# Kernel tuning notes

Measured on AMD Instinct MI355X. Metric: run time of the kernel, lower is better.

## Reference

```python
import jax, jax.numpy as jnp
import numpy as np

B, N, K = 32, 64, 128          # batch, atoms per cell, channel width (128x0e + 128x1o)
R_MAX = 5.0
NUM_BESSEL = 8
P_CUT = 5                       # num_polynomial_cutoff
AVG_NEIGH = 16.0                # avg_num_neighbors
H_MLP = 512                     # hidden_dimensions_size, n_hidden_dimensions = 2
FEAT = 5 * K                    # ((num_interactions-1)*4 + 1) * 128 = 640


def silu(x):
    return x * jax.nn.sigmoid(x)


def _bessel_cutoff(r, mask):
    # Bessel radial basis * polynomial cutoff (MACE), masked on valid edges.
    n = jnp.arange(1, NUM_BESSEL + 1, dtype=r.dtype)
    rb = jnp.sqrt(2.0 / R_MAX) * jnp.sin(n * (jnp.pi / R_MAX) * r[..., None]) / r[..., None]
    u = r / R_MAX
    p = float(P_CUT)
    fc = 1.0 - 0.5 * (p + 1) * (p + 2) * u**P_CUT + p * (p + 2) * u**(P_CUT + 1) - 0.5 * p * (p + 1) * u**(P_CUT + 2)
    fc = fc * (u < 1.0)
    return rb * (fc * mask)[..., None]


def _sph(uvec):
    # Real spherical harmonics l=0,1,2 (component normalization), uvec: unit edge vectors.
    x, y, z = uvec[..., 0], uvec[..., 1], uvec[..., 2]
    s3, s5, s15 = 3.0**0.5, 5.0**0.5, 15.0**0.5
    Y0 = jnp.ones_like(x)[..., None]
    Y1 = jnp.stack([s3 * x, s3 * y, s3 * z], -1)
    Y2 = jnp.stack([s15 * x * y, s15 * y * z, 0.5 * s5 * (3 * z * z - 1.0),
                    s15 * x * z, 0.5 * s15 * (x * x - y * y)], -1)
    return Y0, Y1, Y2


def _radial_mlp(x, w0, b0, w1, b1, w2, b2, w3, b3):
    h = silu(x @ w0 + b0)
    h = silu(h @ w1 + b1)
    h = silu(h @ w2 + b2)
    return h @ w3 + b3


def setup_inputs() -> dict:
    key = jax.random.key(0)
    ks = jax.random.split(key, 32)
    f32 = jnp.float32

    def lin(k, fan_in, shape):
        return (jax.random.normal(k, shape, dtype=f32) / np.sqrt(fan_in)).astype(f32)

    inp = {
        "noisy_relative_positions": jax.random.uniform(ks[0], (B, N, 3), dtype=f32),
        "time": jax.random.uniform(ks[1], (B, 1), dtype=f32),
        "unit_cell": (11.0 * jnp.eye(3, dtype=f32) + 0.3 * jax.random.uniform(ks[2], (B, 3, 3), dtype=f32)),
        "w_embed": lin(ks[3], 1, (K,)),
        # interaction 1 radial MLP: 8 -> 64 -> 64 -> 64 -> 3*K (weights for l=0,1,2 paths)
        "r1_w0": lin(ks[4], NUM_BESSEL, (NUM_BESSEL, 64)), "r1_b0": jnp.zeros((64,), f32),
        "r1_w1": lin(ks[5], 64, (64, 64)), "r1_b1": jnp.zeros((64,), f32),
        "r1_w2": lin(ks[6], 64, (64, 64)), "r1_b2": jnp.zeros((64,), f32),
        "r1_w3": lin(ks[7], 64, (64, 3 * K)), "r1_b3": jnp.zeros((3 * K,), f32),
        "mix1_l0": lin(ks[8], K, (K, K)),
        "mix1_l1": lin(ks[9], K, (K, K)),
        "mix1_l2": lin(ks[10], K, (K, K)),
        # interaction 2 radial MLP: 8 -> 64 -> 64 -> 64 -> 2*K (paths 0e x 0e -> 0e, 1o x 1o -> 0e)
        "r2_w0": lin(ks[11], NUM_BESSEL, (NUM_BESSEL, 64)), "r2_b0": jnp.zeros((64,), f32),
        "r2_w1": lin(ks[12], 64, (64, 64)), "r2_b1": jnp.zeros((64,), f32),
        "r2_w2": lin(ks[13], 64, (64, 64)), "r2_b2": jnp.zeros((64,), f32),
        "r2_w3": lin(ks[14], 64, (64, 2 * K)), "r2_b3": jnp.zeros((2 * K,), f32),
        "mix2": lin(ks[15], K, (K, K)),
        # readout MLP: 641 -> 512 -> 512 -> 3
        "mlp_w0": lin(ks[16], FEAT + 1, (FEAT + 1, H_MLP)), "mlp_b0": jnp.zeros((H_MLP,), f32),
        "mlp_w1": lin(ks[17], H_MLP, (H_MLP, H_MLP)), "mlp_b1": jnp.zeros((H_MLP,), f32),
        "mlp_w2": lin(ks[18], H_MLP, (H_MLP, 3)), "mlp_b2": jnp.zeros((3,), f32),
    }
    return inp


def reference(noisy_relative_positions, time, unit_cell, w_embed,
              r1_w0, r1_b0, r1_w1, r1_b1, r1_w2, r1_b2, r1_w3, r1_b3,
              mix1_l0, mix1_l1, mix1_l2,
              r2_w0, r2_b0, r2_w1, r2_b1, r2_w2, r2_b2, r2_w3, r2_b3, mix2,
              mlp_w0, mlp_b0, mlp_w1, mlp_b1, mlp_w2, mlp_b2):
    frac = noisy_relative_positions                      # [B,N,3] fractional
    d = frac[:, :, None, :] - frac[:, None, :, :]        # [B,N,N,3]
    d = d - jnp.round(d)                                 # minimum-image PBC
    dc = jnp.einsum('bijc,bcd->bijd', d, unit_cell)      # cartesian displacements
    r = jnp.sqrt(jnp.maximum(jnp.sum(dc * dc, -1), 1e-12))
    mask = (r < R_MAX) & (~jnp.eye(N, dtype=bool))[None]
    r_safe = jnp.where(mask, r, 1.0)
    uvec = dc / r_safe[..., None] * mask[..., None]      # unit edge vectors (0 off-edge)

    rad = _bessel_cutoff(r_safe, mask)                   # [B,N,N,8]
    Y0, Y1, Y2 = _sph(uvec)                              # [B,N,N,1|3|5]

    h0 = jnp.broadcast_to(w_embed, (B, N, K))            # element embedding (single species)

    # ---- interaction 1: radial-weighted tensor product h_j (x) Y_l, scatter over j ----
    we = _radial_mlp(rad, r1_w0, r1_b0, r1_w1, r1_b1, r1_w2, r1_b2, r1_w3, r1_b3)
    we = we.reshape(B, N, N, 3, K) * mask[..., None, None]
    hj = h0[:, None, :, :]                               # sender features [B,1,N,K]
    msg0 = jnp.einsum('bijk,bijm->bimk', we[..., 0, :] * hj, Y0)[:, :, 0] / AVG_NEIGH  # [B,N,K]
    msg1 = jnp.einsum('bijk,bijm->bimk', we[..., 1, :] * hj, Y1) / AVG_NEIGH           # [B,N,3,K]
    msg2 = jnp.einsum('bijk,bijm->bimk', we[..., 2, :] * hj, Y2) / AVG_NEIGH           # [B,N,5,K]

    s1 = msg0 @ mix1_l0 + jnp.sum(msg2 * msg2, axis=2) @ mix1_l2   # scalars [B,N,K]
    v1 = jnp.einsum('bimk,kc->bimc', msg1, mix1_l1)                # vectors [B,N,3,K]
    h1 = silu(s1)

    # ---- interaction 2: scalar output from 0e x 0e and 1o x 1o -> 0e paths ----
    we2 = _radial_mlp(rad, r2_w0, r2_b0, r2_w1, r2_b1, r2_w2, r2_b2, r2_w3, r2_b3)
    we2 = we2.reshape(B, N, N, 2, K) * mask[..., None, None]
    msg_a = jnp.sum(we2[..., 0, :] * h1[:, None, :, :], axis=2)    # [B,N,K]
    inv = jnp.einsum('bijm,bjmk->bijk', Y1, v1)                    # Y1 . v1_j invariant
    msg_b = jnp.sum(we2[..., 1, :] * inv, axis=2)
    s2 = ((msg_a + msg_b) / AVG_NEIGH) @ mix2                      # [B,N,K]

    # node_feats: layer1 full irreps (128x0e + 128x1o -> 512) + layer2 scalars (128) = 640
    node_feats = jnp.concatenate([s1, v1.reshape(B, N, 3 * K), s2], axis=-1)

    t = jnp.broadcast_to(time[:, None, :], (B, N, 1))
    x = jnp.concatenate([node_feats, t], axis=-1)                  # [B,N,641]
    x = jax.nn.relu(x @ mlp_w0 + mlp_b0)
    x = jax.nn.relu(x @ mlp_w1 + mlp_b1)
    return x @ mlp_w2 + mlp_b2                                     # [B,N,3]
```

## Files before the change

kernel.cpp:

```cpp
#include <hip/hip_runtime.h>
#include <math.h>

#define B_ 32
#define N_ 64
#define K_ 128
#define NPAIR (B_*N_*N_)
#define PREP_TOTAL 733184

typedef __attribute__((ext_vector_type(8))) short short8;
typedef __attribute__((ext_vector_type(8))) __bf16 bf16x8;
typedef __attribute__((ext_vector_type(4))) float floatx4;

__device__ __forceinline__ float silu_f(float x) {
    return x / (1.0f + expf(-x));
}

__device__ __forceinline__ short f2bf(float x) {
    union { float f; unsigned u; } v; v.f = x;
    unsigned r = (v.u + 0x7FFFu + ((v.u >> 16) & 1u)) >> 16;
    return (short)r;
}
__device__ __forceinline__ float bf2f(short s) {
    union { unsigned u; float f; } v;
    v.u = ((unsigned)(unsigned short)s) << 16;
    return v.f;
}
__device__ __forceinline__ bf16x8 ld_frag(const short* p) {
    short8 r = *(const short8*)p;
    return __builtin_bit_cast(bf16x8, r);
}

__global__ __launch_bounds__(256) void prep_kernel(
    const float* __restrict__ r1w1, const float* __restrict__ r1w2,
    const float* __restrict__ r2w1, const float* __restrict__ r2w2,
    const float* __restrict__ r2w3, const float* __restrict__ mw0,
    const float* __restrict__ mw1,
    const float* __restrict__ r1w0, const float* __restrict__ r2w0,
    const float* __restrict__ r1w3,
    const float* __restrict__ l0, const float* __restrict__ l1,
    const float* __restrict__ l2,
    short* __restrict__ dst)
{
    int idx = blockIdx.x * 256 + threadIdx.x;
    if (idx >= PREP_TOTAL) return;
    short v;
    if (idx < 4096) {
        int h = idx >> 6, k = idx & 63; v = f2bf(r1w1[k*64 + h]);
    } else if (idx < 8192) {
        int i = idx - 4096; int h = i >> 6, k = i & 63; v = f2bf(r1w2[k*64 + h]);
    } else if (idx < 12288) {
        int i = idx - 8192; int h = i >> 6, k = i & 63; v = f2bf(r2w1[k*64 + h]);
    } else if (idx < 16384) {
        int i = idx - 12288; int h = i >> 6, k = i & 63; v = f2bf(r2w2[k*64 + h]);
    } else if (idx < 32768) {
        int i = idx - 16384; int col = i >> 6, h = i & 63; v = f2bf(r2w3[h*256 + col]);
    } else if (idx < 393216) {
        int i = idx - 32768; int n = i / 704, k = i - n*704;
        v = (k < 641) ? f2bf(mw0[(size_t)k*512 + n]) : (short)0;
    } else if (idx < 655360) {
        int i = idx - 393216; int n = i >> 9, k = i & 511;
        v = f2bf(mw1[(size_t)k*512 + n]);
    } else if (idx < 657408) {
        int i = idx - 655360; int h = i >> 5, k = i & 31;
        v = (k < 8) ? f2bf(r1w0[k*64 + h]) : (short)0;
    } else if (idx < 659456) {
        int i = idx - 657408; int h = i >> 5, k = i & 31;
        v = (k < 8) ? f2bf(r2w0[k*64 + h]) : (short)0;
    } else if (idx < 684032) {
        int i = idx - 659456; int col = i >> 6, h = i & 63;
        v = f2bf(r1w3[(size_t)h*384 + col]);
    } else {
        int i = idx - 684032; int n = i >> 7, k = i & 127;
        float src = (n < 128) ? l0[(size_t)k*128 + n]
                  : (n < 256) ? l1[(size_t)k*128 + (n-128)]
                              : l2[(size_t)k*128 + (n-256)];
        v = f2bf(src);
    }
    dst[idx] = v;
}

__global__ __launch_bounds__(256) void geom_kernel(
    const float* __restrict__ pos, const float* __restrict__ cell,
    float* __restrict__ rad, float* __restrict__ Y1, float* __restrict__ Y2,
    float* __restrict__ maskf)
{
    int p = blockIdx.x * 256 + threadIdx.x;
    if (p >= NPAIR) return;
    int b = p >> 12;
    int ij = p & 4095;
    int i = ij >> 6, j = ij & 63;
    const float* pi = pos + (size_t)(b*N_ + i)*3;
    const float* pj = pos + (size_t)(b*N_ + j)*3;
    float d0 = pi[0]-pj[0], d1 = pi[1]-pj[1], d2 = pi[2]-pj[2];
    d0 -= rintf(d0); d1 -= rintf(d1); d2 -= rintf(d2);
    const float* C = cell + b*9;
    float dc0 = d0*C[0] + d1*C[3] + d2*C[6];
    float dc1 = d0*C[1] + d1*C[4] + d2*C[7];
    float dc2 = d0*C[2] + d1*C[5] + d2*C[8];
    float r2 = fmaxf(dc0*dc0 + dc1*dc1 + dc2*dc2, 1e-12f);
    float r = sqrtf(r2);
    bool m = (r < 5.0f) && (i != j);
    float mf = m ? 1.0f : 0.0f;
    float rs = m ? r : 1.0f;
    float inv_rs = 1.0f / rs;
    float x = dc0*inv_rs*mf, y = dc1*inv_rs*mf, z = dc2*inv_rs*mf;
    float u = r * 0.2f;
    float u2 = u*u, u4 = u2*u2, u5 = u4*u;
    float fc = 1.0f - 21.0f*u5 + 35.0f*u5*u - 15.0f*u5*u2;
    fc = (u < 1.0f) ? fc : 0.0f;
    float pref = 0.6324555320336759f * inv_rs * (fc * mf);
    float w = 0.6283185307179586f * rs;
    float sw = sinf(w), cw = cosf(w);
    float twoc = 2.0f * cw;
    float sm = 0.0f, s = sw;
    #pragma unroll
    for (int n = 1; n <= 8; n++) {
        rad[(size_t)p*8 + (n-1)] = pref * s;
        float nx = twoc*s - sm;
        sm = s; s = nx;
    }
    const float s3  = 1.7320508075688772f;
    const float s5  = 2.23606797749979f;
    const float s15 = 3.872983346207417f;
    float* y1 = Y1 + (size_t)p*3;
    y1[0] = s3*x; y1[1] = s3*y; y1[2] = s3*z;
    float* y2 = Y2 + (size_t)p*5;
    y2[0] = s15*x*y;
    y2[1] = s15*y*z;
    y2[2] = 0.5f*s5*(3.0f*z*z - 1.0f);
    y2[3] = s15*x*z;
    y2[4] = 0.5f*s15*(x*x - y*y);
    maskf[p] = mf;
}

__device__ __forceinline__ void mfma_layer(
    const short* __restrict__ src, const short* __restrict__ WT,
    const float* __restrict__ bias, short* __restrict__ dst,
    int wv, int qd, int nn)
{
    floatx4 acc[4];
    #pragma unroll
    for (int tt = 0; tt < 4; tt++) acc[tt] = (floatx4){0.f, 0.f, 0.f, 0.f};
    #pragma unroll
    for (int ks = 0; ks < 64; ks += 32) {
        bf16x8 a = ld_frag(&src[(wv*16 + nn)*72 + ks + qd*8]);
        #pragma unroll
        for (int tt = 0; tt < 4; tt++) {
            bf16x8 b = ld_frag(&WT[(tt*16 + nn)*64 + ks + qd*8]);
            acc[tt] = __builtin_amdgcn_mfma_f32_16x16x32_bf16(a, b, acc[tt], 0, 0, 0);
        }
    }
    #pragma unroll
    for (int tt = 0; tt < 4; tt++) {
        int col = tt*16 + nn;
        float bv = bias[col];
        #pragma unroll
        for (int i = 0; i < 4; i++) {
            int row = wv*16 + qd*4 + i;
            dst[row*72 + col] = f2bf(silu_f(acc[tt][i] + bv));
        }
    }
}

__device__ __forceinline__ void mfma_layer_T(
    const short* __restrict__ src, const short* __restrict__ WT,
    const float* __restrict__ bias, short* __restrict__ dstT,
    int wv, int qd, int nn)
{
    floatx4 acc[4];
    #pragma unroll
    for (int tt = 0; tt < 4; tt++) acc[tt] = (floatx4){0.f, 0.f, 0.f, 0.f};
    #pragma unroll
    for (int ks = 0; ks < 64; ks += 32) {
        bf16x8 a = ld_frag(&src[(wv*16 + nn)*72 + ks + qd*8]);
        #pragma unroll
        for (int tt = 0; tt < 4; tt++) {
            bf16x8 b = ld_frag(&WT[(tt*16 + nn)*64 + ks + qd*8]);
            acc[tt] = __builtin_amdgcn_mfma_f32_16x16x32_bf16(a, b, acc[tt], 0, 0, 0);
        }
    }
    #pragma unroll
    for (int tt = 0; tt < 4; tt++) {
        int col = tt*16 + nn;
        float bv = bias[col];
        #pragma unroll
        for (int i = 0; i < 4; i++) {
            int row = wv*16 + qd*4 + i;
            dstT[col*72 + row] = f2bf(silu_f(acc[tt][i] + bv));
        }
    }
}

__device__ __forceinline__ void mfma_layer0(
    const short* __restrict__ rad_bf, const short* __restrict__ w0T,
    const float* __restrict__ b0, short* __restrict__ dst,
    int wv, int qd, int nn)
{
    floatx4 acc[4];
    #pragma unroll
    for (int tt = 0; tt < 4; tt++) acc[tt] = (floatx4){0.f, 0.f, 0.f, 0.f};
    bf16x8 a = ld_frag(&rad_bf[(wv*16 + nn)*32 + qd*8]);
    #pragma unroll
    for (int tt = 0; tt < 4; tt++) {
        bf16x8 b = ld_frag(&w0T[(tt*16 + nn)*32 + qd*8]);
        acc[tt] = __builtin_amdgcn_mfma_f32_16x16x32_bf16(a, b, acc[tt], 0, 0, 0);
    }
    #pragma unroll
    for (int tt = 0; tt < 4; tt++) {
        int col = tt*16 + nn;
        float bv = b0[col];
        #pragma unroll
        for (int i = 0; i < 4; i++) {
            int row = wv*16 + qd*4 + i;
            dst[row*72 + col] = f2bf(silu_f(acc[tt][i] + bv));
        }
    }
}

__global__ __launch_bounds__(256) void pass1_kernel(
    const float* __restrict__ rad, const float* __restrict__ Y1g,
    const float* __restrict__ Y2g, const float* __restrict__ maskg,
    const float* __restrict__ wemb,
    const short* __restrict__ w0T, const float* __restrict__ b0,
    const short* __restrict__ w1T, const float* __restrict__ b1,
    const short* __restrict__ w2T, const float* __restrict__ b2,
    const short* __restrict__ w3T, const float* __restrict__ b3,
    const short* __restrict__ lcatT, const float* __restrict__ timeg,
    float* __restrict__ h1g, float* __restrict__ v1g, short* __restrict__ featsb)
{
    __shared__ __align__(16) char smem[23040];
    short* actA   = (short*)smem;
    short* actB   = (short*)(smem + 9216);
    float* msg    = (float*)(smem + 9216);
    float* q_s    = (float*)(smem + 9216 + 4608);
    short* rad_bf = (short*)(smem + 18432);
    short* Ym_bf  = (short*)(smem + 18432);
    short* G_bf   = (short*)(smem + 18432 + 2304);
    short* A2     = (short*)smem;
    float* Psa    = (float*)(smem + 9216);
    float* Psb    = Psa + 128;

    int t = threadIdx.x;
    int wv = t >> 6, lane = t & 63, qd = lane >> 4, nn = lane & 15;
    int node = blockIdx.x;
    int b = node >> 6;
    size_t pbase = (size_t)node * 64;

    for (int idx = t; idx < 2048; idx += 256) {
        int j = idx >> 5, k = idx & 31;
        rad_bf[j*32 + k] = (k < 8) ? f2bf(rad[pbase*8 + j*8 + k]) : (short)0;
    }
    float vals[9];
    float sy9[9];
    if (t < 64) {
        int j = t;
        float mf = maskg[pbase + j];
        vals[0] = mf;
        #pragma unroll
        for (int m = 0; m < 3; m++) vals[1+m] = Y1g[(pbase+j)*3 + m] * mf;
        #pragma unroll
        for (int m = 0; m < 5; m++) vals[4+m] = Y2g[(pbase+j)*5 + m] * mf;
        #pragma unroll
        for (int m = 0; m < 9; m++) {
            float s = vals[m];
            #pragma unroll
            for (int off = 32; off > 0; off >>= 1) s += __shfl_xor(s, off);
            sy9[m] = s;
        }
    }
    __syncthreads();

    mfma_layer0(rad_bf, w0T, b0, actA, wv, qd, nn);
    __syncthreads();

    if (t < 64) {
        int j = t;
        #pragma unroll
        for (int m = 0; m < 9; m++) Ym_bf[m*72 + j] = f2bf(vals[m]);
        #pragma unroll
        for (int m = 9; m < 16; m++) Ym_bf[m*72 + j] = 0;
        #pragma unroll
        for (int m = 0; m < 9; m++)
            if (j == m) *(float*)(&Ym_bf[m*72 + 64]) = sy9[m];
    }
    mfma_layer(actA, w1T, b1, actB, wv, qd, nn);
    __syncthreads();

    mfma_layer_T(actB, w2T, b2, actA, wv, qd, nn);
    __syncthreads();

    {
        floatx4 acc = (floatx4){0.f, 0.f, 0.f, 0.f};
        #pragma unroll
        for (int ks = 0; ks < 64; ks += 32) {
            bf16x8 a = ld_frag(&Ym_bf[nn*72 + ks + qd*8]);
            bf16x8 bb = ld_frag(&actA[(wv*16 + nn)*72 + ks + qd*8]);
            acc = __builtin_amdgcn_mfma_f32_16x16x32_bf16(a, bb, acc, 0, 0, 0);
        }
        #pragma unroll
        for (int i = 0; i < 4; i++)
            G_bf[(qd*4 + i)*72 + wv*16 + nn] = f2bf(acc[i]);
    }
    __syncthreads();

    {
        floatx4 acc[6];
        #pragma unroll
        for (int tt = 0; tt < 6; tt++) acc[tt] = (floatx4){0.f, 0.f, 0.f, 0.f};
        #pragma unroll
        for (int ks = 0; ks < 64; ks += 32) {
            bf16x8 a = ld_frag(&G_bf[nn*72 + ks + qd*8]);
            #pragma unroll
            for (int tt = 0; tt < 6; tt++) {
                bf16x8 bb = ld_frag(&w3T[((wv*6 + tt)*16 + nn)*64 + ks + qd*8]);
                acc[tt] = __builtin_amdgcn_mfma_f32_16x16x32_bf16(a, bb, acc[tt], 0, 0, 0);
            }
        }
        #pragma unroll
        for (int tt = 0; tt < 6; tt++) {
            int col = (wv*6 + tt)*16 + nn;
            #pragma unroll
            for (int i = 0; i < 4; i++) {
                int m = qd*4 + i;
                if (m < 9) {
                    int c = (m == 0) ? 0 : ((m < 4) ? 1 : 2);
                    int k = col - c*128;
                    if (k >= 0 && k < 128) {
                        float sym = *(const float*)(&Ym_bf[m*72 + 64]);
                        msg[m*128 + k] = (acc[tt][i] + sym*b3[col]) * wemb[k] * 0.0625f;
                    }
                }
            }
        }
    }
    __syncthreads();

    if (t < 128) {
        int k = t;
        float acc = 0.f;
        #pragma unroll
        for (int m = 4; m < 9; m++) { float v = msg[m*128 + k]; acc += v*v; }
        q_s[k] = acc;
    }
    __syncthreads();

    for (int idx = t; idx < 2048; idx += 256) {
        int r = idx >> 7, k = idx & 127;
        float v = (r == 0) ? msg[k]
                : (r == 1) ? q_s[k]
                : (r < 5)  ? msg[(r-1)*128 + k] : 0.f;
        A2[r*136 + k] = f2bf(v);
    }
    __syncthreads();

    {
        bf16x8 pa[4];
        #pragma unroll
        for (int ksI = 0; ksI < 4; ksI++)
            pa[ksI] = ld_frag(&A2[nn*136 + ksI*32 + qd*8]);
        floatx4 acc[6];
        #pragma unroll
        for (int tt = 0; tt < 6; tt++) acc[tt] = (floatx4){0.f, 0.f, 0.f, 0.f};
        #pragma unroll
        for (int tt = 0; tt < 6; tt++) {
            int tn = wv*6 + tt;
            #pragma unroll
            for (int ksI = 0; ksI < 4; ksI++) {
                bf16x8 bf = ld_frag(&lcatT[((size_t)(tn*16 + nn))*128 + ksI*32 + qd*8]);
                acc[tt] = __builtin_amdgcn_mfma_f32_16x16x32_bf16(pa[ksI], bf, acc[tt], 0, 0, 0);
            }
        }
        #pragma unroll
        for (int tt = 0; tt < 6; tt++) {
            int n = (wv*6 + tt)*16 + nn;
            #pragma unroll
            for (int i = 0; i < 4; i++) {
                int r = qd*4 + i;
                float val = acc[tt][i];
                if (r == 0 && n < 128) Psa[n] = val;
                else if (r == 1 && n >= 256) Psb[n - 256] = val;
                else if (r >= 2 && r < 5 && n >= 128 && n < 256) {
                    int m = r - 2, cc = n - 128;
                    v1g[(size_t)node*384 + m*128 + cc] = val;
                    featsb[(size_t)node*704 + 128 + m*128 + cc] = f2bf(val);
                }
            }
        }
    }
    __syncthreads();

    if (t < 128) {
        float s1 = Psa[t] + Psb[t];
        featsb[(size_t)node*704 + t] = f2bf(s1);
        h1g[(size_t)node*128 + t] = silu_f(s1);
    } else if (t == 128) {
        featsb[(size_t)node*704 + 640] = f2bf(timeg[b]);
    } else if (t > 128 && t < 192) {
        featsb[(size_t)node*704 + 640 + (t - 128)] = 0;
    }
}

__global__ __launch_bounds__(256) void pass2_kernel(
    const float* __restrict__ rad, const float* __restrict__ Y1g,
    const float* __restrict__ maskg,
    const short* __restrict__ w0T, const float* __restrict__ b0,
    const short* __restrict__ w1T, const float* __restrict__ b1,
    const short* __restrict__ w2T, const float* __restrict__ b2,
    const short* __restrict__ w3T, const float* __restrict__ b3,
    const float* __restrict__ mix2,
    const float* __restrict__ h1g, const float* __restrict__ v1g,
    short* __restrict__ featsb)
{
    __shared__ __align__(16) char smem[22528];
    short* actA   = (short*)smem;
    short* actB   = (short*)(smem + 9216);
    short* rad_bf = (short*)(smem + 18432);
    float* aux    = (float*)(smem + 18432);
    float* mask_s = aux;
    float* Y1s    = aux + 64;
    float* msgab  = aux + 320;

    int t = threadIdx.x;
    int wv = t >> 6, lane = t & 63, qd = lane >> 4, nn = lane & 15;
    int node = blockIdx.x;
    int b = node >> 6;
    size_t pbase = (size_t)node * 64;

    for (int idx = t; idx < 2048; idx += 256) {
        int j = idx >> 5, k = idx & 31;
        rad_bf[j*32 + k] = (k < 8) ? f2bf(rad[pbase*8 + j*8 + k]) : (short)0;
    }
    float pmf = 0.f, py0 = 0.f, py1 = 0.f, py2 = 0.f;
    if (t < 64) {
        pmf = maskg[pbase + t];
        py0 = Y1g[(pbase+t)*3 + 0];
        py1 = Y1g[(pbase+t)*3 + 1];
        py2 = Y1g[(pbase+t)*3 + 2];
    }
    __syncthreads();

    mfma_layer0(rad_bf, w0T, b0, actA, wv, qd, nn);
    __syncthreads();

    if (t < 64) {
        mask_s[t] = pmf;
        Y1s[t*4 + 0] = py0; Y1s[t*4 + 1] = py1; Y1s[t*4 + 2] = py2;
    }
    if (t < 128) msgab[t] = 0.f;
    mfma_layer(actA, w1T, b1, actB, wv, qd, nn);
    __syncthreads();

    mfma_layer(actB, w2T, b2, actA, wv, qd, nn);
    __syncthreads();

    for (int g = 0; g < 4; g++) {
        floatx4 acc[4];
        #pragma unroll
        for (int tt = 0; tt < 4; tt++) acc[tt] = (floatx4){0.f, 0.f, 0.f, 0.f};
        #pragma unroll
        for (int ks = 0; ks < 64; ks += 32) {
            bf16x8 a = ld_frag(&actA[(wv*16 + nn)*72 + ks + qd*8]);
            #pragma unroll
            for (int tt = 0; tt < 4; tt++) {
                int col0 = g*64 + tt*16;
                bf16x8 bb = ld_frag(&w3T[(col0 + nn)*64 + ks + qd*8]);
                acc[tt] = __builtin_amdgcn_mfma_f32_16x16x32_bf16(a, bb, acc[tt], 0, 0, 0);
            }
        }
        #pragma unroll
        for (int tt = 0; tt < 4; tt++) {
            int col = g*64 + tt*16 + nn;
            float bias = b3[col];
            int k = col & 127;
            float p = 0.f;
            if (col < 128) {
                #pragma unroll
                for (int i = 0; i < 4; i++) {
                    int j = wv*16 + qd*4 + i;
                    float we = (acc[tt][i] + bias) * mask_s[j];
                    p += we * h1g[((size_t)b*64 + j)*128 + k];
                }
            } else {
                #pragma unroll
                for (int i = 0; i < 4; i++) {
                    int j = wv*16 + qd*4 + i;
                    float we = (acc[tt][i] + bias) * mask_s[j];
                    const float* vb = &v1g[((size_t)b*64 + j)*384 + k];
                    float inv = Y1s[j*4+0]*vb[0] + Y1s[j*4+1]*vb[128] + Y1s[j*4+2]*vb[256];
                    p += we * inv;
                }
            }
            p += __shfl_xor(p, 16);
            p += __shfl_xor(p, 32);
            if (qd == 0) atomicAdd(&msgab[k], p);
        }
    }
    __syncthreads();

    if (t < 128) {
        int c = t;
        float acc = 0.f;
        for (int k = 0; k < 128; k++) acc += msgab[k] * mix2[k*128 + c];
        featsb[(size_t)node*704 + 512 + c] = f2bf(acc * 0.0625f);
    }
}

__global__ __launch_bounds__(256) void gemm_mfma_kernel(
    const short* __restrict__ A, int lda,
    const short* __restrict__ BT, int ldb, int K,
    const float* __restrict__ bias, short* __restrict__ Cout, int ldo)
{
    __shared__ short As[64*72];
    __shared__ short Bs[64*72];
    int t = threadIdx.x;
    int wv = t >> 6, lane = t & 63, qd = lane >> 4, nn = lane & 15;
    int m0 = blockIdx.x * 64, n0 = blockIdx.y * 64;
    floatx4 acc[4];
    #pragma unroll
    for (int tt = 0; tt < 4; tt++) acc[tt] = (floatx4){0.f, 0.f, 0.f, 0.f};

    for (int kc = 0; kc < K; kc += 64) {
        for (int s = t; s < 512; s += 256) {
            int j = s >> 3, kk = (s & 7) * 8;
            *(uint4*)&As[j*72 + kk] = *(const uint4*)&A[(size_t)(m0 + j)*lda + kc + kk];
            *(uint4*)&Bs[j*72 + kk] = *(const uint4*)&BT[(size_t)(n0 + j)*ldb + kc + kk];
        }
        __syncthreads();
        #pragma unroll
        for (int ks = 0; ks < 64; ks += 32) {
            bf16x8 a = ld_frag(&As[(wv*16 + nn)*72 + ks + qd*8]);
            #pragma unroll
            for (int tt = 0; tt < 4; tt++) {
                bf16x8 bb = ld_frag(&Bs[(tt*16 + nn)*72 + ks + qd*8]);
                acc[tt] = __builtin_amdgcn_mfma_f32_16x16x32_bf16(a, bb, acc[tt], 0, 0, 0);
            }
        }
        __syncthreads();
    }
    #pragma unroll
    for (int tt = 0; tt < 4; tt++) {
        int n = n0 + tt*16 + nn;
        float bv = bias[n];
        #pragma unroll
        for (int i = 0; i < 4; i++) {
            int m = m0 + wv*16 + qd*4 + i;
            Cout[(size_t)m*ldo + n] = f2bf(fmaxf(acc[tt][i] + bv, 0.f));
        }
    }
}

__global__ __launch_bounds__(64) void final3_kernel(
    const short* __restrict__ H, const float* __restrict__ w2,
    const float* __restrict__ b2, float* __restrict__ out)
{
    int node = blockIdx.x, lane = threadIdx.x;
    float a0 = 0.f, a1 = 0.f, a2 = 0.f;
    #pragma unroll
    for (int r = 0; r < 8; r++) {
        int k = r*64 + lane;
        float h = bf2f(H[(size_t)node*512 + k]);
        a0 += h * w2[k*3 + 0];
        a1 += h * w2[k*3 + 1];
        a2 += h * w2[k*3 + 2];
    }
    #pragma unroll
    for (int off = 32; off > 0; off >>= 1) {
        a0 += __shfl_down(a0, off);
        a1 += __shfl_down(a1, off);
        a2 += __shfl_down(a2, off);
    }
    if (lane == 0) {
        out[(size_t)node*3 + 0] = a0 + b2[0];
        out[(size_t)node*3 + 1] = a1 + b2[1];
        out[(size_t)node*3 + 2] = a2 + b2[2];
    }
}

extern "C" void kernel_launch(void* const* d_in, const int* in_sizes, int n_in,
                              void* d_out, int out_size, void* d_ws, size_t ws_size,
                              hipStream_t stream) {
    const float* pos   = (const float*)d_in[0];
    const float* timeg = (const float*)d_in[1];
    const float* cell  = (const float*)d_in[2];
    const float* wemb  = (const float*)d_in[3];
    const float* r1w0  = (const float*)d_in[4];
    const float* r1b0  = (const float*)d_in[5];
    const float* r1w1  = (const float*)d_in[6];
    const float* r1b1  = (const float*)d_in[7];
    const float* r1w2  = (const float*)d_in[8];
    const float* r1b2  = (const float*)d_in[9];
    const float* r1w3  = (const float*)d_in[10];
    const float* r1b3  = (const float*)d_in[11];
    const float* l0    = (const float*)d_in[12];
    const float* l1    = (const float*)d_in[13];
    const float* l2    = (const float*)d_in[14];
    const float* r2w0  = (const float*)d_in[15];
    const float* r2b0  = (const float*)d_in[16];
    const float* r2w1  = (const float*)d_in[17];
    const float* r2b1  = (const float*)d_in[18];
    const float* r2w2  = (const float*)d_in[19];
    const float* r2b2  = (const float*)d_in[20];
    const float* r2w3  = (const float*)d_in[21];
    const float* r2b3  = (const float*)d_in[22];
    const float* mix2  = (const float*)d_in[23];
    const float* mw0   = (const float*)d_in[24];
    const float* mb0   = (const float*)d_in[25];
    const float* mw1   = (const float*)d_in[26];
    const float* mb1   = (const float*)d_in[27];
    const float* mw2   = (const float*)d_in[28];
    const float* mb2   = (const float*)d_in[29];

    float* ws    = (float*)d_ws;
    float* rad   = ws;
    float* Y1    = rad   + (size_t)NPAIR*8;
    float* Y2    = Y1    + (size_t)NPAIR*3;
    float* maskf = Y2    + (size_t)NPAIR*5;
    float* h1    = maskf + (size_t)NPAIR;
    float* v1    = h1    + (size_t)B_*N_*K_;
    short* featsb = (short*)(v1 + (size_t)B_*N_*3*K_);
    short* prep  = featsb + (size_t)2048*704;
    short* w1T_1 = prep;
    short* w2T_1 = prep + 4096;
    short* w1T_2 = prep + 8192;
    short* w2T_2 = prep + 12288;
    short* w3T_2 = prep + 16384;
    short* wT0   = prep + 32768;
    short* wT1   = prep + 393216;
    short* w0T_1 = prep + 655360;
    short* w0T_2 = prep + 657408;
    short* w3T_1 = prep + 659456;
    short* lcatT = prep + 684032;
    short* h0bb = (short*)rad;
    short* h1bb = (short*)Y2;

    prep_kernel<<<(PREP_TOTAL + 255)/256, 256, 0, stream>>>(
        r1w1, r1w2, r2w1, r2w2, r2w3, mw0, mw1,
        r1w0, r2w0, r1w3, l0, l1, l2, prep);
    geom_kernel<<<NPAIR/256, 256, 0, stream>>>(pos, cell, rad, Y1, Y2, maskf);
    pass1_kernel<<<B_*N_, 256, 0, stream>>>(rad, Y1, Y2, maskf, wemb,
        w0T_1, r1b0, w1T_1, r1b1, w2T_1, r1b2, w3T_1, r1b3, lcatT, timeg,
        h1, v1, featsb);
    pass2_kernel<<<B_*N_, 256, 0, stream>>>(rad, Y1, maskf,
        w0T_2, r2b0, w1T_2, r2b1, w2T_2, r2b2, w3T_2, r2b3, mix2, h1, v1, featsb);
    dim3 g0(32, 8);
    gemm_mfma_kernel<<<g0, 256, 0, stream>>>(featsb, 704, wT0, 704, 704, mb0, h0bb, 512);
    gemm_mfma_kernel<<<g0, 256, 0, stream>>>(h0bb, 512, wT1, 512, 512, mb1, h1bb, 512);
    final3_kernel<<<B_*N_, 64, 0, stream>>>(h1bb, mw2, mb2, (float*)d_out);
}
```

Baseline: 290.2 us.

## Process two nodes per block with two waves each, reusing weight fragments

```diff
diff --git a/kernel.cpp b/kernel.cpp
--- a/kernel.cpp
+++ b/kernel.cpp
@@ -133,88 +133,74 @@
     maskf[p] = mf;
 }
 
-__device__ __forceinline__ void mfma_layer(
+template<int TR>
+__device__ __forceinline__ void mfma_layer2(
     const short* __restrict__ src, const short* __restrict__ WT,
     const float* __restrict__ bias, short* __restrict__ dst,
-    int wv, int qd, int nn)
-{
-    floatx4 acc[4];
-    #pragma unroll
-    for (int tt = 0; tt < 4; tt++) acc[tt] = (floatx4){0.f, 0.f, 0.f, 0.f};
+    int u, int qd, int nn)
+{
+    floatx4 acc[2][4];
+    #pragma unroll
+    for (int r = 0; r < 2; r++)
+        #pragma unroll
+        for (int tt = 0; tt < 4; tt++) acc[r][tt] = (floatx4){0.f, 0.f, 0.f, 0.f};
     #pragma unroll
     for (int ks = 0; ks < 64; ks += 32) {
-        bf16x8 a = ld_frag(&src[(wv*16 + nn)*72 + ks + qd*8]);
+        bf16x8 a0 = ld_frag(&src[((u*2+0)*16 + nn)*72 + ks + qd*8]);
+        bf16x8 a1 = ld_frag(&src[((u*2+1)*16 + nn)*72 + ks + qd*8]);
         #pragma unroll
         for (int tt = 0; tt < 4; tt++) {
             bf16x8 b = ld_frag(&WT[(tt*16 + nn)*64 + ks + qd*8]);
-            acc[tt] = __builtin_amdgcn_mfma_f32_16x16x32_bf16(a, b, acc[tt], 0, 0, 0);
-        }
-    }
-    #pragma unroll
-    for (int tt = 0; tt < 4; tt++) {
-        int col = tt*16 + nn;
-        float bv = bias[col];
-        #pragma unroll
-        for (int i = 0; i < 4; i++) {
-            int row = wv*16 + qd*4 + i;
-            dst[row*72 + col] = f2bf(silu_f(acc[tt][i] + bv));
-        }
-    }
-}
-
-__device__ __forceinline__ void mfma_layer_T(
-    const short* __restrict__ src, const short* __restrict__ WT,
-    const float* __restrict__ bias, short* __restrict__ dstT,
-    int wv, int qd, int nn)
-{
-    floatx4 acc[4];
-    #pragma unroll
-    for (int tt = 0; tt < 4; tt++) acc[tt] = (floatx4){0.f, 0.f, 0.f, 0.f};
-    #pragma unroll
-    for (int ks = 0; ks < 64; ks += 32) {
-        bf16x8 a = ld_frag(&src[(wv*16 + nn)*72 + ks + qd*8]);
+            acc[0][tt] = __builtin_amdgcn_mfma_f32_16x16x32_bf16(a0, b, acc[0][tt], 0, 0, 0);
+            acc[1][tt] = __builtin_amdgcn_mfma_f32_16x16x32_bf16(a1, b, acc[1][tt], 0, 0, 0);
+        }
+    }
+    #pragma unroll
+    for (int r = 0; r < 2; r++)
         #pragma unroll
         for (int tt = 0; tt < 4; tt++) {
-            bf16x8 b = ld_frag(&WT[(tt*16 + nn)*64 + ks + qd*8]);
-            acc[tt] = __builtin_amdgcn_mfma_f32_16x16x32_bf16(a, b, acc[tt], 0, 0, 0);
-        }
-    }
-    #pragma unroll
-    for (int tt = 0; tt < 4; tt++) {
-        int col = tt*16 + nn;
-        float bv = bias[col];
-        #pragma unroll
-        for (int i = 0; i < 4; i++) {
-            int row = wv*16 + qd*4 + i;
-            dstT[col*72 + row] = f2bf(silu_f(acc[tt][i] + bv));
-        }
-    }
-}
-
-__device__ __forceinline__ void mfma_layer0(
+            int col = tt*16 + nn;
+            float bv = bias[col];
+            #pragma unroll
+            for (int i = 0; i < 4; i++) {
+                int row = (u*2+r)*16 + qd*4 + i;
+                float v = silu_f(acc[r][tt][i] + bv);
+                if (TR) dst[col*72 + row] = f2bf(v);
+                else    dst[row*72 + col] = f2bf(v);
+            }
+        }
+}
+
+__device__ __forceinline__ void mfma_layer0_2(
     const short* __restrict__ rad_bf, const short* __restrict__ w0T,
     const float* __restrict__ b0, short* __restrict__ dst,
-    int wv, int qd, int nn)
-{
-    floatx4 acc[4];
-    #pragma unroll
-    for (int tt = 0; tt < 4; tt++) acc[tt] = (floatx4){0.f, 0.f, 0.f, 0.f};
-    bf16x8 a = ld_frag(&rad_bf[(wv*16 + nn)*32 + qd*8]);
+    int u, int qd, int nn)
+{
+    floatx4 acc[2][4];
+    #pragma unroll
+    for (int r = 0; r < 2; r++)
+        #pragma unroll
+        for (int tt = 0; tt < 4; tt++) acc[r][tt] = (floatx4){0.f, 0.f, 0.f, 0.f};
+    bf16x8 a0 = ld_frag(&rad_bf[((u*2+0)*16 + nn)*32 + qd*8]);
+    bf16x8 a1 = ld_frag(&rad_bf[((u*2+1)*16 + nn)*32 + qd*8]);
     #pragma unroll
     for (int tt = 0; tt < 4; tt++) {
         bf16x8 b = ld_frag(&w0T[(tt*16 + nn)*32 + qd*8]);
-        acc[tt] = __builtin_amdgcn_mfma_f32_16x16x32_bf16(a, b, acc[tt], 0, 0, 0);
-    }
-    #pragma unroll
-    for (int tt = 0; tt < 4; tt++) {
-        int col = tt*16 + nn;
-        float bv = b0[col];
-        #pragma unroll
-        for (int i = 0; i < 4; i++) {
-            int row = wv*16 + qd*4 + i;
-            dst[row*72 + col] = f2bf(silu_f(acc[tt][i] + bv));
-        }
-    }
+        acc[0][tt] = __builtin_amdgcn_mfma_f32_16x16x32_bf16(a0, b, acc[0][tt], 0, 0, 0);
+        acc[1][tt] = __builtin_amdgcn_mfma_f32_16x16x32_bf16(a1, b, acc[1][tt], 0, 0, 0);
+    }
+    #pragma unroll
+    for (int r = 0; r < 2; r++)
+        #pragma unroll
+        for (int tt = 0; tt < 4; tt++) {
+            int col = tt*16 + nn;
+            float bv = b0[col];
+            #pragma unroll
+            for (int i = 0; i < 4; i++) {
+                int row = (u*2+r)*16 + qd*4 + i;
+                dst[row*72 + col] = f2bf(silu_f(acc[r][tt][i] + bv));
+            }
+        }
 }
 
 __global__ __launch_bounds__(256) void pass1_kernel(
@@ -228,32 +214,35 @@
     const short* __restrict__ lcatT, const float* __restrict__ timeg,
     float* __restrict__ h1g, float* __restrict__ v1g, short* __restrict__ featsb)
 {
-    __shared__ __align__(16) char smem[23040];
-    short* actA   = (short*)smem;
-    short* actB   = (short*)(smem + 9216);
-    float* msg    = (float*)(smem + 9216);
-    float* q_s    = (float*)(smem + 9216 + 4608);
-    short* rad_bf = (short*)(smem + 18432);
-    short* Ym_bf  = (short*)(smem + 18432);
-    short* G_bf   = (short*)(smem + 18432 + 2304);
-    short* A2     = (short*)smem;
-    float* Psa    = (float*)(smem + 9216);
-    float* Psb    = Psa + 128;
-
+    __shared__ __align__(16) char smem[46080];
     int t = threadIdx.x;
     int wv = t >> 6, lane = t & 63, qd = lane >> 4, nn = lane & 15;
-    int node = blockIdx.x;
+    int ln = wv >> 1;
+    int u  = wv & 1;
+    int tl = t & 127;
+    int node = blockIdx.x*2 + ln;
     int b = node >> 6;
     size_t pbase = (size_t)node * 64;
 
-    for (int idx = t; idx < 2048; idx += 256) {
+    char* base = smem + ln*23040;
+    short* actA   = (short*)base;
+    short* actB   = (short*)(base + 9216);
+    float* msg2f  = (float*)(base + 9216);
+    short* rad_bf = (short*)(base + 18432);
+    short* Ym_bf  = (short*)(base + 18432);
+    short* G_bf   = (short*)(base + 18432 + 2304);
+    short* A2     = (short*)base;
+    float* Psa    = (float*)(base + 9216);
+    float* Psb    = Psa + 128;
+
+    for (int idx = tl; idx < 2048; idx += 128) {
         int j = idx >> 5, k = idx & 31;
         rad_bf[j*32 + k] = (k < 8) ? f2bf(rad[pbase*8 + j*8 + k]) : (short)0;
     }
     float vals[9];
     float sy9[9];
-    if (t < 64) {
-        int j = t;
+    if (tl < 64) {
+        int j = tl;
         float mf = maskg[pbase + j];
         vals[0] = mf;
         #pragma unroll
@@ -270,11 +259,11 @@
     }
     __syncthreads();
 
-    mfma_layer0(rad_bf, w0T, b0, actA, wv, qd, nn);
-    __syncthreads();
-
-    if (t < 64) {
-        int j = t;
+    mfma_layer0_2(rad_bf, w0T, b0, actA, u, qd, nn);
+    __syncthreads();
+
+    if (tl < 64) {
+        int j = tl;
         #pragma unroll
         for (int m = 0; m < 9; m++) Ym_bf[m*72 + j] = f2bf(vals[m]);
         #pragma unroll
@@ -283,51 +272,62 @@
         for (int m = 0; m < 9; m++)
             if (j == m) *(float*)(&Ym_bf[m*72 + 64]) = sy9[m];
     }
-    mfma_layer(actA, w1T, b1, actB, wv, qd, nn);
-    __syncthreads();
-
-    mfma_layer_T(actB, w2T, b2, actA, wv, qd, nn);
+    mfma_layer2<0>(actA, w1T, b1, actB, u, qd, nn);
+    __syncthreads();
+
+    mfma_layer2<1>(actB, w2T, b2, actA, u, qd, nn);
     __syncthreads();
 
     {
-        floatx4 acc = (floatx4){0.f, 0.f, 0.f, 0.f};
-        #pragma unroll
-        for (int ks = 0; ks < 64; ks += 32) {
-            bf16x8 a = ld_frag(&Ym_bf[nn*72 + ks + qd*8]);
-            bf16x8 bb = ld_frag(&actA[(wv*16 + nn)*72 + ks + qd*8]);
-            acc = __builtin_amdgcn_mfma_f32_16x16x32_bf16(a, bb, acc, 0, 0, 0);
-        }
-        #pragma unroll
-        for (int i = 0; i < 4; i++)
-            G_bf[(qd*4 + i)*72 + wv*16 + nn] = f2bf(acc[i]);
+        bf16x8 ya0 = ld_frag(&Ym_bf[nn*72 + qd*8]);
+        bf16x8 ya1 = ld_frag(&Ym_bf[nn*72 + 32 + qd*8]);
+        #pragma unroll
+        for (int hh = 0; hh < 2; hh++) {
+            int ht = u*2 + hh;
+            floatx4 acc = (floatx4){0.f, 0.f, 0.f, 0.f};
+            bf16x8 b0f = ld_frag(&actA[(ht*16 + nn)*72 + qd*8]);
+            bf16x8 b1f = ld_frag(&actA[(ht*16 + nn)*72 + 32 + qd*8]);
+            acc = __builtin_amdgcn_mfma_f32_16x16x32_bf16(ya0, b0f, acc, 0, 0, 0);
+            acc = __builtin_amdgcn_mfma_f32_16x16x32_bf16(ya1, b1f, acc, 0, 0, 0);
+            #pragma unroll
+            for (int i = 0; i < 4; i++)
+                G_bf[(qd*4 + i)*72 + ht*16 + nn] = f2bf(acc[i]);
+        }
     }
     __syncthreads();
 
     {
-        floatx4 acc[6];
-        #pragma unroll
-        for (int tt = 0; tt < 6; tt++) acc[tt] = (floatx4){0.f, 0.f, 0.f, 0.f};
-        #pragma unroll
-        for (int ks = 0; ks < 64; ks += 32) {
-            bf16x8 a = ld_frag(&G_bf[nn*72 + ks + qd*8]);
+        bf16x8 ga0 = ld_frag(&G_bf[nn*72 + qd*8]);
+        bf16x8 ga1 = ld_frag(&G_bf[nn*72 + 32 + qd*8]);
+        #pragma unroll
+        for (int g2 = 0; g2 < 2; g2++) {
+            floatx4 acc[6];
+            #pragma unroll
+            for (int tt = 0; tt < 6; tt++) acc[tt] = (floatx4){0.f, 0.f, 0.f, 0.f};
             #pragma unroll
             for (int tt = 0; tt < 6; tt++) {
-                bf16x8 bb = ld_frag(&w3T[((wv*6 + tt)*16 + nn)*64 + ks + qd*8]);
-                acc[tt] = __builtin_amdgcn_mfma_f32_16x16x32_bf16(a, bb, acc[tt], 0, 0, 0);
-            }
-        }
-        #pragma unroll
-        for (int tt = 0; tt < 6; tt++) {
-            int col = (wv*6 + tt)*16 + nn;
-            #pragma unroll
-            for (int i = 0; i < 4; i++) {
-                int m = qd*4 + i;
-                if (m < 9) {
-                    int c = (m == 0) ? 0 : ((m < 4) ? 1 : 2);
-                    int k = col - c*128;
-                    if (k >= 0 && k < 128) {
-                        float sym = *(const float*)(&Ym_bf[m*72 + 64]);
-                        msg[m*128 + k] = (acc[tt][i] + sym*b3[col]) * wemb[k] * 0.0625f;
+                int tn = u*12 + g2*6 + tt;
+                bf16x8 b0f = ld_frag(&w3T[(tn*16 + nn)*64 + qd*8]);
+                bf16x8 b1f = ld_frag(&w3T[(tn*16 + nn)*64 + 32 + qd*8]);
+                acc[tt] = __builtin_amdgcn_mfma_f32_16x16x32_bf16(ga0, b0f, acc[tt], 0, 0, 0);
+                acc[tt] = __builtin_amdgcn_mfma_f32_16x16x32_bf16(ga1, b1f, acc[tt], 0, 0, 0);
+            }
+            #pragma unroll
+            for (int tt = 0; tt < 6; tt++) {
+                int col = (u*12 + g2*6 + tt)*16 + nn;
+                #pragma unroll
+                for (int i = 0; i < 4; i++) {
+                    int m = qd*4 + i;
+                    if (m < 9) {
+                        int c = (m == 0) ? 0 : ((m < 4) ? 1 : 2);
+                        int k = col - c*128;
+                        if (k >= 0 && k < 128) {
+                            float sym = *(const float*)(&Ym_bf[m*72 + 64]);
+                            float val = (acc[tt][i] + sym*b3[col]) * wemb[k] * 0.0625f;
+                            if (m == 0)      A2[k] = f2bf(val);
+                            else if (m < 4)  A2[(m+1)*136 + k] = f2bf(val);
+                            else             msg2f[(m-4)*128 + k] = val;
+                        }
                     }
                 }
             }
@@ -335,21 +335,16 @@
     }
     __syncthreads();
 
-    if (t < 128) {
-        int k = t;
+    if (tl < 128) {
+        int k = tl;
         float acc = 0.f;
         #pragma unroll
-        for (int m = 4; m < 9; m++) { float v = msg[m*128 + k]; acc += v*v; }
-        q_s[k] = acc;
-    }
-    __syncthreads();
-
-    for (int idx = t; idx < 2048; idx += 256) {
-        int r = idx >> 7, k = idx & 127;
-        float v = (r == 0) ? msg[k]
-                : (r == 1) ? q_s[k]
-                : (r < 5)  ? msg[(r-1)*128 + k] : 0.f;
-        A2[r*136 + k] = f2bf(v);
+        for (int m = 0; m < 5; m++) { float v = msg2f[m*128 + k]; acc += v*v; }
+        A2[136 + k] = f2bf(acc);
+    }
+    for (int z = tl; z < 1408; z += 128) {
+        int r = 5 + (z >> 7), k = z & 127;
+        A2[r*136 + k] = 0;
     }
     __syncthreads();
 
@@ -358,45 +353,48 @@
         #pragma unroll
         for (int ksI = 0; ksI < 4; ksI++)
             pa[ksI] = ld_frag(&A2[nn*136 + ksI*32 + qd*8]);
-        floatx4 acc[6];
-        #pragma unroll
-        for (int tt = 0; tt < 6; tt++) acc[tt] = (floatx4){0.f, 0.f, 0.f, 0.f};
-        #pragma unroll
-        for (int tt = 0; tt < 6; tt++) {
-            int tn = wv*6 + tt;
-            #pragma unroll
-            for (int ksI = 0; ksI < 4; ksI++) {
-                bf16x8 bf = ld_frag(&lcatT[((size_t)(tn*16 + nn))*128 + ksI*32 + qd*8]);
-                acc[tt] = __builtin_amdgcn_mfma_f32_16x16x32_bf16(pa[ksI], bf, acc[tt], 0, 0, 0);
-            }
-        }
-        #pragma unroll
-        for (int tt = 0; tt < 6; tt++) {
-            int n = (wv*6 + tt)*16 + nn;
-            #pragma unroll
-            for (int i = 0; i < 4; i++) {
-                int r = qd*4 + i;
-                float val = acc[tt][i];
-                if (r == 0 && n < 128) Psa[n] = val;
-                else if (r == 1 && n >= 256) Psb[n - 256] = val;
-                else if (r >= 2 && r < 5 && n >= 128 && n < 256) {
-                    int m = r - 2, cc = n - 128;
-                    v1g[(size_t)node*384 + m*128 + cc] = val;
-                    featsb[(size_t)node*704 + 128 + m*128 + cc] = f2bf(val);
+        #pragma unroll
+        for (int g2 = 0; g2 < 2; g2++) {
+            floatx4 acc[6];
+            #pragma unroll
+            for (int tt = 0; tt < 6; tt++) acc[tt] = (floatx4){0.f, 0.f, 0.f, 0.f};
+            #pragma unroll
+            for (int tt = 0; tt < 6; tt++) {
+                int tn = u*12 + g2*6 + tt;
+                #pragma unroll
+                for (int ksI = 0; ksI < 4; ksI++) {
+                    bf16x8 bf = ld_frag(&lcatT[((size_t)(tn*16 + nn))*128 + ksI*32 + qd*8]);
+                    acc[tt] = __builtin_amdgcn_mfma_f32_16x16x32_bf16(pa[ksI], bf, acc[tt], 0, 0, 0);
                 }
             }
-        }
-    }
-    __syncthreads();
-
-    if (t < 128) {
-        float s1 = Psa[t] + Psb[t];
-        featsb[(size_t)node*704 + t] = f2bf(s1);
-        h1g[(size_t)node*128 + t] = silu_f(s1);
-    } else if (t == 128) {
-        featsb[(size_t)node*704 + 640] = f2bf(timeg[b]);
-    } else if (t > 128 && t < 192) {
-        featsb[(size_t)node*704 + 640 + (t - 128)] = 0;
+            #pragma unroll
+            for (int tt = 0; tt < 6; tt++) {
+                int n = (u*12 + g2*6 + tt)*16 + nn;
+                #pragma unroll
+                for (int i = 0; i < 4; i++) {
+                    int r = qd*4 + i;
+                    float val = acc[tt][i];
+                    if (r == 0 && n < 128) Psa[n] = val;
+                    else if (r == 1 && n >= 256) Psb[n - 256] = val;
+                    else if (r >= 2 && r < 5 && n >= 128 && n < 256) {
+                        int m = r - 2, cc = n - 128;
+                        v1g[(size_t)node*384 + m*128 + cc] = val;
+                        featsb[(size_t)node*704 + 128 + m*128 + cc] = f2bf(val);
+                    }
+                }
+            }
+        }
+    }
+    __syncthreads();
+
+    if (tl < 128) {
+        float s1 = Psa[tl] + Psb[tl];
+        featsb[(size_t)node*704 + tl] = f2bf(s1);
+        h1g[(size_t)node*128 + tl] = silu_f(s1);
+    }
+    if (tl >= 64 && tl < 128) {
+        int c = 640 + (tl - 64);
+        featsb[(size_t)node*704 + c] = (tl == 64) ? f2bf(timeg[b]) : (short)0;
     }
 }
 
@@ -411,94 +409,112 @@
     const float* __restrict__ h1g, const float* __restrict__ v1g,
     short* __restrict__ featsb)
 {
-    __shared__ __align__(16) char smem[22528];
-    short* actA   = (short*)smem;
-    short* actB   = (short*)(smem + 9216);
-    short* rad_bf = (short*)(smem + 18432);
-    float* aux    = (float*)(smem + 18432);
+    __shared__ __align__(16) char smem[45056];
+    int t = threadIdx.x;
+    int wv = t >> 6, lane = t & 63, qd = lane >> 4, nn = lane & 15;
+    int ln = wv >> 1, u = wv & 1, tl = t & 127;
+    int node = blockIdx.x*2 + ln;
+    int b = node >> 6;
+    size_t pbase = (size_t)node * 64;
+
+    char* base = smem + ln*22528;
+    short* actA   = (short*)base;
+    short* actB   = (short*)(base + 9216);
+    short* rad_bf = (short*)(base + 18432);
+    float* aux    = (float*)(base + 18432);
     float* mask_s = aux;
     float* Y1s    = aux + 64;
     float* msgab  = aux + 320;
 
-    int t = threadIdx.x;
-    int wv = t >> 6, lane = t & 63, qd = lane >> 4, nn = lane & 15;
-    int node = blockIdx.x;
-    int b = node >> 6;
-    size_t pbase = (size_t)node * 64;
-
-    for (int idx = t; idx < 2048; idx += 256) {
+    for (int idx = tl; idx < 2048; idx += 128) {
         int j = idx >> 5, k = idx & 31;
         rad_bf[j*32 + k] = (k < 8) ? f2bf(rad[pbase*8 + j*8 + k]) : (short)0;
     }
     float pmf = 0.f, py0 = 0.f, py1 = 0.f, py2 = 0.f;
-    if (t < 64) {
-        pmf = maskg[pbase + t];
-        py0 = Y1g[(pbase+t)*3 + 0];
-        py1 = Y1g[(pbase+t)*3 + 1];
-        py2 = Y1g[(pbase+t)*3 + 2];
-    }
-    __syncthreads();
-
-    mfma_layer0(rad_bf, w0T, b0, actA, wv, qd, nn);
-    __syncthreads();
-
-    if (t < 64) {
-        mask_s[t] = pmf;
-        Y1s[t*4 + 0] = py0; Y1s[t*4 + 1] = py1; Y1s[t*4 + 2] = py2;
-    }
-    if (t < 128) msgab[t] = 0.f;
-    mfma_layer(actA, w1T, b1, actB, wv, qd, nn);
-    __syncthreads();
-
-    mfma_layer(actB, w2T, b2, actA, wv, qd, nn);
-    __syncthreads();
-
-    for (int g = 0; g < 4; g++) {
-        floatx4 acc[4];
-        #pragma unroll
-        for (int tt = 0; tt < 4; tt++) acc[tt] = (floatx4){0.f, 0.f, 0.f, 0.f};
-        #pragma unroll
-        for (int ks = 0; ks < 64; ks += 32) {
-            bf16x8 a = ld_frag(&actA[(wv*16 + nn)*72 + ks + qd*8]);
+    if (tl < 64) {
+        pmf = maskg[pbase + tl];
+        py0 = Y1g[(pbase+tl)*3 + 0];
+        py1 = Y1g[(pbase+tl)*3 + 1];
+        py2 = Y1g[(pbase+tl)*3 + 2];
+    }
+    __syncthreads();
+
+    mfma_layer0_2(rad_bf, w0T, b0, actA, u, qd, nn);
+    __syncthreads();
+
+    if (tl < 64) {
+        mask_s[tl] = pmf;
+        Y1s[tl*4 + 0] = py0; Y1s[tl*4 + 1] = py1; Y1s[tl*4 + 2] = py2;
+    }
+    if (tl < 128) { if (tl < 128) msgab[tl & 127] = 0.f; }
+    mfma_layer2<0>(actA, w1T, b1, actB, u, qd, nn);
+    __syncthreads();
+
+    mfma_layer2<0>(actB, w2T, b2, actA, u, qd, nn);
+    __syncthreads();
+
+    {
+        bf16x8 af[2][2];
+        #pragma unroll
+        for (int r = 0; r < 2; r++) {
+            int rt = u*2 + r;
+            af[r][0] = ld_frag(&actA[(rt*16 + nn)*72 + qd*8]);
+            af[r][1] = ld_frag(&actA[(rt*16 + nn)*72 + 32 + qd*8]);
+        }
+        for (int cg = 0; cg < 4; cg++) {
+            floatx4 acc[2][4];
+            #pragma unroll
+            for (int r = 0; r < 2; r++)
+                #pragma unroll
+                for (int tt = 0; tt < 4; tt++) acc[r][tt] = (floatx4){0.f, 0.f, 0.f, 0.f};
             #pragma unroll
             for (int tt = 0; tt < 4; tt++) {
-                int col0 = g*64 + tt*16;
-                bf16x8 bb = ld_frag(&w3T[(col0 + nn)*64 + ks + qd*8]);
-                acc[tt] = __builtin_amdgcn_mfma_f32_16x16x32_bf16(a, bb, acc[tt], 0, 0, 0);
-            }
-        }
-        #pragma unroll
-        for (int tt = 0; tt < 4; tt++) {
-            int col = g*64 + tt*16 + nn;
-            float bias = b3[col];
-            int k = col & 127;
-            float p = 0.f;
-            if (col < 128) {
+                int ct = cg*4 + tt;
+                bf16x8 b0f = ld_frag(&w3T[(ct*16 + nn)*64 + qd*8]);
+                bf16x8 b1f = ld_frag(&w3T[(ct*16 + nn)*64 + 32 + qd*8]);
                 #pragma unroll
-                for (int i = 0; i < 4; i++) {
-                    int j = wv*16 + qd*4 + i;
-                    float we = (acc[tt][i] + bias) * mask_s[j];
-                    p += we * h1g[((size_t)b*64 + j)*128 + k];
+                for (int r = 0; r < 2; r++) {
+                    acc[r][tt] = __builtin_amdgcn_mfma_f32_16x16x32_bf16(af[r][0], b0f, acc[r][tt], 0, 0, 0);
+                    acc[r][tt] = __builtin_amdgcn_mfma_f32_16x16x32_bf16(af[r][1], b1f, acc[r][tt], 0, 0, 0);
                 }
-            } else {
+            }
+            #pragma unroll
+            for (int r = 0; r < 2; r++) {
+                int rt = u*2 + r;
                 #pragma unroll
-                for (int i = 0; i < 4; i++) {
-                    int j = wv*16 + qd*4 + i;
-                    float we = (acc[tt][i] + bias) * mask_s[j];
-                    const float* vb = &v1g[((size_t)b*64 + j)*384 + k];
-                    float inv = Y1s[j*4+0]*vb[0] + Y1s[j*4+1]*vb[128] + Y1s[j*4+2]*vb[256];
-                    p += we * inv;
+                for (int tt = 0; tt < 4; tt++) {
+                    int col = (cg*4 + tt)*16 + nn;
+                    float bias = b3[col];
+                    int k = col & 127;
+                    float p = 0.f;
+                    if (col < 128) {
+                        #pragma unroll
+                        for (int i = 0; i < 4; i++) {
+                            int j = rt*16 + qd*4 + i;
+                            float we = (acc[r][tt][i] + bias) * mask_s[j];
+                            p += we * h1g[((size_t)b*64 + j)*128 + k];
+                        }
+                    } else {
+                        #pragma unroll
+                        for (int i = 0; i < 4; i++) {
+                            int j = rt*16 + qd*4 + i;
+                            float we = (acc[r][tt][i] + bias) * mask_s[j];
+                            const float* vb = &v1g[((size_t)b*64 + j)*384 + k];
+                            float inv = Y1s[j*4+0]*vb[0] + Y1s[j*4+1]*vb[128] + Y1s[j*4+2]*vb[256];
+                            p += we * inv;
+                        }
+                    }
+                    p += __shfl_xor(p, 16);
+                    p += __shfl_xor(p, 32);
+                    if (qd == 0) atomicAdd(&msgab[k], p);
                 }
             }
-            p += __shfl_xor(p, 16);
-            p += __shfl_xor(p, 32);
-            if (qd == 0) atomicAdd(&msgab[k], p);
-        }
-    }
-    __syncthreads();
-
-    if (t < 128) {
-        int c = t;
+        }
+    }
+    __syncthreads();
+
+    if (tl < 128) {
+        int c = tl;
         float acc = 0.f;
         for (int k = 0; k < 128; k++) acc += msgab[k] * mix2[k*128 + c];
         featsb[(size_t)node*704 + 512 + c] = f2bf(acc * 0.0625f);
@@ -637,10 +653,10 @@
         r1w1, r1w2, r2w1, r2w2, r2w3, mw0, mw1,
         r1w0, r2w0, r1w3, l0, l1, l2, prep);
     geom_kernel<<<NPAIR/256, 256, 0, stream>>>(pos, cell, rad, Y1, Y2, maskf);
-    pass1_kernel<<<B_*N_, 256, 0, stream>>>(rad, Y1, Y2, maskf, wemb,
+    pass1_kernel<<<B_*N_/2, 256, 0, stream>>>(rad, Y1, Y2, maskf, wemb,
         w0T_1, r1b0, w1T_1, r1b1, w2T_1, r1b2, w3T_1, r1b3, lcatT, timeg,
         h1, v1, featsb);
-    pass2_kernel<<<B_*N_, 256, 0, stream>>>(rad, Y1, maskf,
+    pass2_kernel<<<B_*N_/2, 256, 0, stream>>>(rad, Y1, maskf,
         w0T_2, r2b0, w1T_2, r2b1, w2T_2, r2b2, w3T_2, r2b3, mix2, h1, v1, featsb);
     dim3 g0(32, 8);
     gemm_mfma_kernel<<<g0, 256, 0, stream>>>(featsb, 704, wT0, 704, 704, mb0, h0bb, 512);
```

Result: no change. 287.5 us (-0.9%).
